# Optimization experiments

Hardware: AMD Instinct MI355X
Metric: run time of the kernel (lower is better)

The kernel has to match this reference:

```python
import jax, jax.numpy as jnp
import numpy as np

N, K, DIM = 65536, 32, 64


def setup_inputs() -> dict:
    key = jax.random.key(0)
    k1, k2, k3, k4 = jax.random.split(key, 4)
    x = jax.random.normal(k1, (N, DIM), jnp.float32)
    log_pi = jax.random.normal(k2, (K, 1), jnp.float32)
    mu = jax.random.normal(k3, (K, DIM), jnp.float32)
    log_sigma_ = jax.random.normal(k4, (K, DIM, DIM), jnp.float32) / 100.0
    return {"x": x, "log_pi": log_pi, "mu": mu, "log_sigma_": log_sigma_}


def reference(x, log_pi, mu, log_sigma_):
    k, d = mu.shape
    # Faithful to torch: softmax over the size-1 last axis of (K,1) -> all ones.
    pi = jax.nn.softmax(log_pi, axis=-1)  # (K, 1)
    # scale_tril construction: strict lower triangle kept, diagonal -> exp(diag) + 1e-3
    diag = jnp.exp(jnp.diagonal(log_sigma_, axis1=-2, axis2=-1)) + 1e-3  # (K, d)
    L = jnp.tril(log_sigma_, -1) + jnp.eye(d, dtype=x.dtype) * diag[:, None, :]  # (K, d, d)
    # batched MVN log_prob via triangular solve
    diff = x[:, None, :] - mu[None, :, :]            # (N, K, d)
    b = jnp.transpose(diff, (1, 2, 0))               # (K, d, N)
    z = jax.scipy.linalg.solve_triangular(L, b, lower=True)  # (K, d, N)
    maha = jnp.sum(z * z, axis=1)                    # (K, N)
    logdet = jnp.sum(jnp.log(diag), axis=-1)         # (K,)
    logp = -0.5 * (maha + d * jnp.log(2.0 * jnp.pi)) - logdet[:, None]  # (K, N)
    p = jnp.exp(logp).T                              # (N, K)
    return jnp.log(jnp.matmul(p, pi).squeeze())      # (N,)
```

## Files before the change

### kernel.cpp

```cpp
#include <hip/hip_runtime.h>

#define KK 32
#define DD 64
#define NB 65536
#define PAD 68
#define FRAGS 12
#define SLOT (FRAGS * 64)
#define MREF 103.0f

typedef __attribute__((ext_vector_type(8))) short bf16x8;
typedef __attribute__((ext_vector_type(4))) float f32x4;

__device__ inline short f2bf(float f) {
  uint32_t u = __builtin_bit_cast(uint32_t, f);
  uint32_t r = (u + 0x7fffu + ((u >> 16) & 1u)) >> 16;
  return (short)(r & 0xffffu);
}
__device__ inline float bf2f(short h) {
  uint32_t u = ((uint32_t)(unsigned short)h) << 16;
  return __builtin_bit_cast(float, u);
}
__device__ inline uint4 pack8(const short* v) {
  uint4 u;
  u.x = (uint32_t)(unsigned short)v[0] | ((uint32_t)(unsigned short)v[1] << 16);
  u.y = (uint32_t)(unsigned short)v[2] | ((uint32_t)(unsigned short)v[3] << 16);
  u.z = (uint32_t)(unsigned short)v[4] | ((uint32_t)(unsigned short)v[5] << 16);
  u.w = (uint32_t)(unsigned short)v[6] | ((uint32_t)(unsigned short)v[7] << 16);
  return u;
}

__global__ __launch_bounds__(64) void md_prep(const float* __restrict__ ls,
                                              const float* __restrict__ mu,
                                              uint4* __restrict__ Bp,
                                              float* __restrict__ Cc,
                                              float* __restrict__ Kc) {
  __shared__ float Ls[DD * DD];
  __shared__ float Ys[DD * PAD];
  const int k = blockIdx.x, j = threadIdx.x;
  const float* __restrict__ lsk = ls + (size_t)k * DD * DD;

#pragma unroll
  for (int it = 0; it < 16; ++it) {
    const int off = it * 256 + j * 4;
    *(float4*)&Ls[off] = *(const float4*)&lsk[off];
  }
  __syncthreads();

  const float dj = expf(Ls[j * DD + j]) + 1e-3f;
  const float invdj = 1.0f / dj;
  {
    float l = logf(dj);
#pragma unroll
    for (int off = 32; off > 0; off >>= 1) l += __shfl_down(l, off, 64);
    if (j == 0) Kc[k] = fmaf(-0.5f, 64.0f * 1.83787706640934534f, -l);
  }

  float z[DD];
#pragma unroll
  for (int i = 0; i < DD; ++i) {
    float s0 = 0.f, s1 = 0.f, s2 = 0.f, s3 = 0.f;
    int m = 0;
#pragma unroll
    for (; m + 4 <= i; m += 4) {
      const float4 lv = *(const float4*)&Ls[i * DD + m];
      s0 = fmaf(lv.x, z[m + 0], s0);
      s1 = fmaf(lv.y, z[m + 1], s1);
      s2 = fmaf(lv.z, z[m + 2], s2);
      s3 = fmaf(lv.w, z[m + 3], s3);
    }
#pragma unroll
    for (; m < i; ++m) s0 = fmaf(Ls[i * DD + m], z[m], s0);
    const float s = (s0 + s1) + (s2 + s3);
    const float di = __shfl(invdj, i, 64);
    z[i] = (i == j) ? invdj : -s * di;
  }

#pragma unroll
  for (int i = 0; i < DD; ++i) Ys[i * PAD + j] = z[i];
  __syncthreads();

  {
    const float* __restrict__ mk = mu + k * DD;
    float c0 = 0.f, c1 = 0.f, c2 = 0.f, c3 = 0.f;
#pragma unroll
    for (int m = 0; m < DD; m += 4) {
      c0 = fmaf(Ys[j * PAD + m + 0], mk[m + 0], c0);
      c1 = fmaf(Ys[j * PAD + m + 1], mk[m + 1], c1);
      c2 = fmaf(Ys[j * PAD + m + 2], mk[m + 2], c2);
      c3 = fmaf(Ys[j * PAD + m + 3], mk[m + 3], c3);
    }
    Cc[k * DD + j] = (c0 + c1) + (c2 + c3);
  }

  const int col = j & 15, q = j >> 4;
  uint4* slot = Bp + (size_t)k * SLOT;
#pragma unroll
  for (int s = 0; s < 2; ++s) {
#pragma unroll
    for (int ct = 0; ct < 4; ++ct) {
      if (s == 1 && ct < 2) continue;
      const int i = col + 16 * ct;
      const float4 v0 = *(const float4*)&Ys[i * PAD + s * 32 + q * 8];
      const float4 v1 = *(const float4*)&Ys[i * PAD + s * 32 + q * 8 + 4];
      const float f[8] = {v0.x, v0.y, v0.z, v0.w, v1.x, v1.y, v1.z, v1.w};
      short hh[8], ll[8];
#pragma unroll
      for (int jj = 0; jj < 8; ++jj) {
        const short h = f2bf(f[jj]);
        hh[jj] = h;
        ll[jj] = f2bf(f[jj] - bf2f(h));
      }
      const int fi = 2 * ct + (s ? 4 : 0);
      slot[(fi + 0) * 64 + j] = pack8(hh);
      slot[(fi + 1) * 64 + j] = pack8(ll);
    }
  }
}

__global__ __launch_bounds__(256, 2) void md_main(const float* __restrict__ x,
                                                  const uint4* __restrict__ Bp,
                                                  const float* __restrict__ Cc,
                                                  const float* __restrict__ Kc,
                                                  float* __restrict__ P) {
  const int tid = threadIdx.x, lane = tid & 63, w = tid >> 6;
  const int quarter = blockIdx.x & 3;
  const int sblk = blockIdx.x >> 2;
  const int base = sblk * 256 + w * 64;
  const int k0 = quarter * 8;
  const int col = lane & 15, q = lane >> 4;

  bf16x8 Xh[4][2], Xl[4][2];
#pragma unroll
  for (int Bt = 0; Bt < 4; ++Bt) {
#pragma unroll
    for (int s = 0; s < 2; ++s) {
      const float* src = x + (size_t)(base + Bt * 16 + col) * DD + s * 32 + q * 8;
      const float4 v0 = *(const float4*)src;
      const float4 v1 = *(const float4*)(src + 4);
      const float f[8] = {v0.x, v0.y, v0.z, v0.w, v1.x, v1.y, v1.z, v1.w};
      bf16x8 h, l;
#pragma unroll
      for (int jj = 0; jj < 8; ++jj) {
        const short hb = f2bf(f[jj]);
        h[jj] = hb;
        l[jj] = f2bf(f[jj] - bf2f(hb));
      }
      Xh[Bt][s] = h;
      Xl[Bt][s] = l;
    }
  }

  const uint4* __restrict__ Bl = Bp + (size_t)k0 * SLOT + lane;

  uint4 F0[FRAGS], F1[FRAGS];
#pragma unroll
  for (int fi = 0; fi < FRAGS; ++fi) F0[fi] = Bl[fi * 64];

  float run_s[4] = {0.f, 0.f, 0.f, 0.f};

#pragma unroll
  for (int kk = 0; kk < 8; ++kk) {
    const int k = k0 + kk;
    const uint4* cur = (kk & 1) ? F1 : F0;
    uint4* nxt = (kk & 1) ? F0 : F1;
    if (kk < 7) {
      const uint4* __restrict__ src = Bl + (size_t)(kk + 1) * SLOT;
#pragma unroll
      for (int fi = 0; fi < FRAGS; ++fi) nxt[fi] = src[fi * 64];
    }
    const float kc = Kc[k];

    f32x4 mah[4];
#pragma unroll
    for (int Bt = 0; Bt < 4; ++Bt) mah[Bt] = (f32x4){0.f, 0.f, 0.f, 0.f};

#pragma unroll
    for (int ct = 0; ct < 4; ++ct) {
      const bf16x8 A0h = __builtin_bit_cast(bf16x8, cur[2 * ct + 0]);
      const bf16x8 A0l = __builtin_bit_cast(bf16x8, cur[2 * ct + 1]);
      bf16x8 A1h{}, A1l{};
      if (ct >= 2) {
        A1h = __builtin_bit_cast(bf16x8, cur[2 * ct + 4]);
        A1l = __builtin_bit_cast(bf16x8, cur[2 * ct + 5]);
      }
      const f32x4 ci = -*(const f32x4*)&Cc[k * DD + ct * 16 + q * 4];
#pragma unroll
      for (int Bt = 0; Bt < 4; ++Bt) {
        f32x4 z1 = ci;
        z1 = __builtin_amdgcn_mfma_f32_16x16x32_bf16(A0h, Xh[Bt][0], z1, 0, 0, 0);
        z1 = __builtin_amdgcn_mfma_f32_16x16x32_bf16(A0l, Xh[Bt][0], z1, 0, 0, 0);
        z1 = __builtin_amdgcn_mfma_f32_16x16x32_bf16(A0h, Xl[Bt][0], z1, 0, 0, 0);
        if (ct >= 2) {
          f32x4 z2 = (f32x4){0.f, 0.f, 0.f, 0.f};
          z2 = __builtin_amdgcn_mfma_f32_16x16x32_bf16(A1h, Xh[Bt][1], z2, 0, 0, 0);
          z2 = __builtin_amdgcn_mfma_f32_16x16x32_bf16(A1l, Xh[Bt][1], z2, 0, 0, 0);
          z2 = __builtin_amdgcn_mfma_f32_16x16x32_bf16(A1h, Xl[Bt][1], z2, 0, 0, 0);
          z1 += z2;
        }
        mah[Bt] += z1 * z1;
      }
    }

#pragma unroll
    for (int Bt = 0; Bt < 4; ++Bt) {
      float s = (mah[Bt][0] + mah[Bt][1]) + (mah[Bt][2] + mah[Bt][3]);
      s += __shfl_xor(s, 16, 64);
      s += __shfl_xor(s, 32, 64);
      const float t = fmaf(-0.5f, s, kc);
      run_s[Bt] += __expf(t + MREF);
    }
  }

  if (q == 0) {
#pragma unroll
    for (int Bt = 0; Bt < 4; ++Bt) {
      const int sid = base + Bt * 16 + col;
      P[quarter * NB + sid] = run_s[Bt];
    }
  }
}

__global__ __launch_bounds__(256) void md_comb(const float* __restrict__ P,
                                               float* __restrict__ out) {
  const int n = blockIdx.x * 256 + threadIdx.x;
  const float S = (P[n] + P[NB + n]) + (P[2 * NB + n] + P[3 * NB + n]);
  out[n] = logf(S) - MREF;
}

extern "C" void kernel_launch(void* const* d_in, const int* in_sizes, int n_in,
                              void* d_out, int out_size, void* d_ws, size_t ws_size,
                              hipStream_t stream) {
  const float* x  = (const float*)d_in[0];
  const float* mu = (const float*)d_in[2];
  const float* ls = (const float*)d_in[3];
  float* out = (float*)d_out;

  char* ws = (char*)d_ws;
  uint4* Bp = (uint4*)ws;
  float* Cc = (float*)(ws + (size_t)KK * SLOT * 16);
  float* Kc = Cc + KK * DD;
  float* P  = Kc + KK;

  md_prep<<<KK, DD, 0, stream>>>(ls, mu, Bp, Cc, Kc);
  md_main<<<1024, 256, 0, stream>>>(x, Bp, Cc, Kc, P);
  md_comb<<<NB / 256, 256, 0, stream>>>(P, out);
}
```

Before: 122.2 us.

## Fuse combine into main via atomic counter, expand Mahalanobis with cross term

The separate combine kernel is removed. The last of the four quarter-blocks per sample tile, found through an atomic counter, now sums the partials and writes the log. The mean term is moved out of the per-component MFMA accumulation: a precomputed W = L^-T L^-1 mu cross term is computed once per tile with MFMA, and a constant absorbs mu'Sigma^-1 mu. The prep kernel is widened to 256 threads with a 4-way split of the triangular solve, and waves stagger the order in which they visit components. This removes one launch and the Cc loads, but adds atomics, fences, shuffles, and a cancellation risk in the expanded quadratic form.

New measurement: 268.2 us. +119.5%, slower.

```diff
diff --git a/kernel.cpp b/kernel.cpp
--- a/kernel.cpp
+++ b/kernel.cpp
@@ -29,99 +29,128 @@
   return u;
 }
 
-__global__ __launch_bounds__(64) void md_prep(const float* __restrict__ ls,
-                                              const float* __restrict__ mu,
-                                              uint4* __restrict__ Bp,
-                                              float* __restrict__ Cc,
-                                              float* __restrict__ Kc) {
+__global__ __launch_bounds__(256) void md_prep(const float* __restrict__ ls,
+                                               const float* __restrict__ mu,
+                                               uint4* __restrict__ Bp,
+                                               short* __restrict__ Whp,
+                                               short* __restrict__ Wlp,
+                                               float* __restrict__ Kc2,
+                                               int* __restrict__ cnt) {
   __shared__ float Ls[DD * DD];
   __shared__ float Ys[DD * PAD];
-  const int k = blockIdx.x, j = threadIdx.x;
+  __shared__ float invdL[DD];
+  __shared__ float muL[DD];
+  __shared__ float cL[DD];
+  const int k = blockIdx.x, t = threadIdx.x;
+  const int j = t >> 2, sub = t & 3;
   const float* __restrict__ lsk = ls + (size_t)k * DD * DD;
 
 #pragma unroll
-  for (int it = 0; it < 16; ++it) {
-    const int off = it * 256 + j * 4;
-    *(float4*)&Ls[off] = *(const float4*)&lsk[off];
-  }
-  __syncthreads();
-
-  const float dj = expf(Ls[j * DD + j]) + 1e-3f;
-  const float invdj = 1.0f / dj;
+  for (int it = 0; it < 4; ++it) {
+    const int o = (it * 256 + t) * 4;
+    *(float4*)&Ls[o] = *(const float4*)&lsk[o];
+  }
+  if (t < DD) muL[t] = mu[k * DD + t];
+  __syncthreads();
+  if (t < DD) invdL[t] = 1.0f / (expf(Ls[t * DD + t]) + 1e-3f);
+  __syncthreads();
+
+  const float invdj = invdL[j];
+  float z[16];
+#pragma unroll
+  for (int mi = 0; mi < 16; ++mi) z[mi] = 0.f;
+#pragma unroll
+  for (int i = 0; i < DD; ++i) {
+    float p = 0.f;
+#pragma unroll
+    for (int mi = 0; mi < 16; ++mi) {
+      if (4 * mi < i) {
+        const int m = 4 * mi + sub;
+        p = fmaf(Ls[i * DD + m], (m < i) ? z[mi] : 0.f, p);
+      }
+    }
+    p += __shfl_xor(p, 1, 64);
+    p += __shfl_xor(p, 2, 64);
+    const float zi = (i == j) ? invdj : -p * invdL[i];
+    if (sub == (i & 3)) z[i >> 2] = zi;
+  }
+#pragma unroll
+  for (int mi = 0; mi < 16; ++mi) Ys[(4 * mi + sub) * PAD + j] = z[mi];
+  __syncthreads();
+
   {
-    float l = logf(dj);
-#pragma unroll
-    for (int off = 32; off > 0; off >>= 1) l += __shfl_down(l, off, 64);
-    if (j == 0) Kc[k] = fmaf(-0.5f, 64.0f * 1.83787706640934534f, -l);
-  }
-
-  float z[DD];
-#pragma unroll
-  for (int i = 0; i < DD; ++i) {
-    float s0 = 0.f, s1 = 0.f, s2 = 0.f, s3 = 0.f;
-    int m = 0;
-#pragma unroll
-    for (; m + 4 <= i; m += 4) {
-      const float4 lv = *(const float4*)&Ls[i * DD + m];
-      s0 = fmaf(lv.x, z[m + 0], s0);
-      s1 = fmaf(lv.y, z[m + 1], s1);
-      s2 = fmaf(lv.z, z[m + 2], s2);
-      s3 = fmaf(lv.w, z[m + 3], s3);
-    }
-#pragma unroll
-    for (; m < i; ++m) s0 = fmaf(Ls[i * DD + m], z[m], s0);
-    const float s = (s0 + s1) + (s2 + s3);
-    const float di = __shfl(invdj, i, 64);
-    z[i] = (i == j) ? invdj : -s * di;
-  }
-
-#pragma unroll
-  for (int i = 0; i < DD; ++i) Ys[i * PAD + j] = z[i];
+    float p = 0.f;
+#pragma unroll
+    for (int mi = 0; mi < 16; ++mi) {
+      const int m = 4 * mi + sub;
+      p = fmaf(Ys[j * PAD + m], muL[m], p);
+    }
+    p += __shfl_xor(p, 1, 64);
+    p += __shfl_xor(p, 2, 64);
+    if (sub == 0) cL[j] = p;
+  }
   __syncthreads();
 
   {
-    const float* __restrict__ mk = mu + k * DD;
-    float c0 = 0.f, c1 = 0.f, c2 = 0.f, c3 = 0.f;
-#pragma unroll
-    for (int m = 0; m < DD; m += 4) {
-      c0 = fmaf(Ys[j * PAD + m + 0], mk[m + 0], c0);
-      c1 = fmaf(Ys[j * PAD + m + 1], mk[m + 1], c1);
-      c2 = fmaf(Ys[j * PAD + m + 2], mk[m + 2], c2);
-      c3 = fmaf(Ys[j * PAD + m + 3], mk[m + 3], c3);
-    }
-    Cc[k * DD + j] = (c0 + c1) + (c2 + c3);
-  }
-
-  const int col = j & 15, q = j >> 4;
-  uint4* slot = Bp + (size_t)k * SLOT;
-#pragma unroll
-  for (int s = 0; s < 2; ++s) {
-#pragma unroll
-    for (int ct = 0; ct < 4; ++ct) {
-      if (s == 1 && ct < 2) continue;
-      const int i = col + 16 * ct;
-      const float4 v0 = *(const float4*)&Ys[i * PAD + s * 32 + q * 8];
-      const float4 v1 = *(const float4*)&Ys[i * PAD + s * 32 + q * 8 + 4];
-      const float f[8] = {v0.x, v0.y, v0.z, v0.w, v1.x, v1.y, v1.z, v1.w};
-      short hh[8], ll[8];
-#pragma unroll
-      for (int jj = 0; jj < 8; ++jj) {
-        const short h = f2bf(f[jj]);
-        hh[jj] = h;
-        ll[jj] = f2bf(f[jj] - bf2f(h));
-      }
-      const int fi = 2 * ct + (s ? 4 : 0);
-      slot[(fi + 0) * 64 + j] = pack8(hh);
-      slot[(fi + 1) * 64 + j] = pack8(ll);
-    }
-  }
+    float p = 0.f;
+#pragma unroll
+    for (int ii = 0; ii < 16; ++ii) {
+      const int i = 4 * ii + sub;
+      p = fmaf(Ys[i * PAD + j], cL[i], p);
+    }
+    p += __shfl_xor(p, 1, 64);
+    p += __shfl_xor(p, 2, 64);
+    if (sub == 0) {
+      const short h = f2bf(p);
+      Whp[k * DD + j] = h;
+      Wlp[k * DD + j] = f2bf(p - bf2f(h));
+    }
+  }
+
+  if (t < DD) {
+    float r = -logf(invdL[t]) + 0.5f * cL[t] * cL[t];
+#pragma unroll
+    for (int off = 32; off > 0; off >>= 1) r += __shfl_down(r, off, 64);
+    if (t == 0) Kc2[k] = MREF - 0.5f * (64.0f * 1.83787706640934534f) - r;
+  }
+
+  if (t < DD) {
+    const int colp = t & 15, qp = t >> 4;
+    uint4* slot = Bp + (size_t)k * SLOT;
+#pragma unroll
+    for (int s = 0; s < 2; ++s) {
+#pragma unroll
+      for (int ct = 0; ct < 4; ++ct) {
+        if (s == 1 && ct < 2) continue;
+        const int i = colp + 16 * ct;
+        const float4 v0 = *(const float4*)&Ys[i * PAD + s * 32 + qp * 8];
+        const float4 v1 = *(const float4*)&Ys[i * PAD + s * 32 + qp * 8 + 4];
+        const float f[8] = {v0.x, v0.y, v0.z, v0.w, v1.x, v1.y, v1.z, v1.w};
+        short hh[8], ll[8];
+#pragma unroll
+        for (int jj = 0; jj < 8; ++jj) {
+          const short h = f2bf(f[jj]);
+          hh[jj] = h;
+          ll[jj] = f2bf(f[jj] - bf2f(h));
+        }
+        const int fi = 2 * ct + (s ? 4 : 0);
+        slot[(fi + 0) * 64 + t] = pack8(hh);
+        slot[(fi + 1) * 64 + t] = pack8(ll);
+      }
+    }
+  }
+  if (k == 0) cnt[t] = 0;
 }
 
 __global__ __launch_bounds__(256, 2) void md_main(const float* __restrict__ x,
                                                   const uint4* __restrict__ Bp,
-                                                  const float* __restrict__ Cc,
-                                                  const float* __restrict__ Kc,
-                                                  float* __restrict__ P) {
+                                                  const short* __restrict__ Whp,
+                                                  const short* __restrict__ Wlp,
+                                                  const float* __restrict__ Kc2,
+                                                  float* __restrict__ P,
+                                                  int* __restrict__ cnt,
+                                                  float* __restrict__ out) {
+  __shared__ int sOld;
   const int tid = threadIdx.x, lane = tid & 63, w = tid >> 6;
   const int quarter = blockIdx.x & 3;
   const int sblk = blockIdx.x >> 2;
@@ -150,25 +179,54 @@
     }
   }
 
-  const uint4* __restrict__ Bl = Bp + (size_t)k0 * SLOT + lane;
+  f32x4 crossD[4];
+  {
+    bf16x8 WhF[2], WlF[2];
+    const int rr = col & 7;
+#pragma unroll
+    for (int s = 0; s < 2; ++s) {
+      const size_t off = (size_t)(k0 + rr) * DD + s * 32 + q * 8;
+      uint4 hv = *(const uint4*)(Whp + off);
+      uint4 lv = *(const uint4*)(Wlp + off);
+      if (col >= 8) { hv = (uint4){0, 0, 0, 0}; lv = (uint4){0, 0, 0, 0}; }
+      WhF[s] = __builtin_bit_cast(bf16x8, hv);
+      WlF[s] = __builtin_bit_cast(bf16x8, lv);
+    }
+#pragma unroll
+    for (int Bt = 0; Bt < 4; ++Bt) {
+      f32x4 zc = (f32x4){0.f, 0.f, 0.f, 0.f};
+      zc = __builtin_amdgcn_mfma_f32_16x16x32_bf16(WhF[0], Xh[Bt][0], zc, 0, 0, 0);
+      zc = __builtin_amdgcn_mfma_f32_16x16x32_bf16(WlF[0], Xh[Bt][0], zc, 0, 0, 0);
+      zc = __builtin_amdgcn_mfma_f32_16x16x32_bf16(WhF[0], Xl[Bt][0], zc, 0, 0, 0);
+      zc = __builtin_amdgcn_mfma_f32_16x16x32_bf16(WhF[1], Xh[Bt][1], zc, 0, 0, 0);
+      zc = __builtin_amdgcn_mfma_f32_16x16x32_bf16(WlF[1], Xh[Bt][1], zc, 0, 0, 0);
+      zc = __builtin_amdgcn_mfma_f32_16x16x32_bf16(WhF[1], Xl[Bt][1], zc, 0, 0, 0);
+      crossD[Bt] = zc;
+    }
+  }
+
+  const int r0 = (w & 1) * 4;
+  const uint4* __restrict__ Bq = Bp + (size_t)k0 * SLOT + lane;
 
   uint4 F0[FRAGS], F1[FRAGS];
 #pragma unroll
-  for (int fi = 0; fi < FRAGS; ++fi) F0[fi] = Bl[fi * 64];
+  for (int fi = 0; fi < FRAGS; ++fi) F0[fi] = Bq[(size_t)r0 * SLOT + fi * 64];
 
   float run_s[4] = {0.f, 0.f, 0.f, 0.f};
 
 #pragma unroll
   for (int kk = 0; kk < 8; ++kk) {
-    const int k = k0 + kk;
+    const int kkr = (kk + r0) & 7;
+    const int k = k0 + kkr;
     const uint4* cur = (kk & 1) ? F1 : F0;
     uint4* nxt = (kk & 1) ? F0 : F1;
     if (kk < 7) {
-      const uint4* __restrict__ src = Bl + (size_t)(kk + 1) * SLOT;
+      const int kn = (kk + 1 + r0) & 7;
+      const uint4* __restrict__ src = Bq + (size_t)kn * SLOT;
 #pragma unroll
       for (int fi = 0; fi < FRAGS; ++fi) nxt[fi] = src[fi * 64];
     }
-    const float kc = Kc[k];
+    const float kc = Kc2[k];
 
     f32x4 mah[4];
 #pragma unroll
@@ -183,10 +241,9 @@
         A1h = __builtin_bit_cast(bf16x8, cur[2 * ct + 4]);
         A1l = __builtin_bit_cast(bf16x8, cur[2 * ct + 5]);
       }
-      const f32x4 ci = -*(const f32x4*)&Cc[k * DD + ct * 16 + q * 4];
 #pragma unroll
       for (int Bt = 0; Bt < 4; ++Bt) {
-        f32x4 z1 = ci;
+        f32x4 z1 = (f32x4){0.f, 0.f, 0.f, 0.f};
         z1 = __builtin_amdgcn_mfma_f32_16x16x32_bf16(A0h, Xh[Bt][0], z1, 0, 0, 0);
         z1 = __builtin_amdgcn_mfma_f32_16x16x32_bf16(A0l, Xh[Bt][0], z1, 0, 0, 0);
         z1 = __builtin_amdgcn_mfma_f32_16x16x32_bf16(A0h, Xl[Bt][0], z1, 0, 0, 0);
@@ -201,30 +258,38 @@
       }
     }
 
+    const int half16 = ((kk >> 2) + (w & 1)) & 1;
 #pragma unroll
     for (int Bt = 0; Bt < 4; ++Bt) {
       float s = (mah[Bt][0] + mah[Bt][1]) + (mah[Bt][2] + mah[Bt][3]);
       s += __shfl_xor(s, 16, 64);
       s += __shfl_xor(s, 32, 64);
-      const float t = fmaf(-0.5f, s, kc);
-      run_s[Bt] += __expf(t + MREF);
+      const float cv = __shfl(crossD[Bt][kk & 3], half16 * 16 + col, 64);
+      const float tt = fmaf(-0.5f, s, kc + cv);
+      run_s[Bt] += __expf(tt);
     }
   }
 
   if (q == 0) {
 #pragma unroll
-    for (int Bt = 0; Bt < 4; ++Bt) {
-      const int sid = base + Bt * 16 + col;
-      P[quarter * NB + sid] = run_s[Bt];
-    }
-  }
-}
-
-__global__ __launch_bounds__(256) void md_comb(const float* __restrict__ P,
-                                               float* __restrict__ out) {
-  const int n = blockIdx.x * 256 + threadIdx.x;
-  const float S = (P[n] + P[NB + n]) + (P[2 * NB + n] + P[3 * NB + n]);
-  out[n] = logf(S) - MREF;
+    for (int Bt = 0; Bt < 4; ++Bt)
+      __hip_atomic_store(&P[quarter * NB + base + Bt * 16 + col], run_s[Bt],
+                         __ATOMIC_RELAXED, __HIP_MEMORY_SCOPE_AGENT);
+  }
+  __threadfence();
+  __syncthreads();
+  if (tid == 0) sOld = atomicAdd(&cnt[sblk], 1);
+  __syncthreads();
+  if (sOld == 3) {
+    __threadfence();
+    const int n = sblk * 256 + tid;
+    float S = 0.f;
+#pragma unroll
+    for (int qq = 0; qq < 4; ++qq)
+      S += __hip_atomic_load(&P[qq * NB + n], __ATOMIC_RELAXED,
+                             __HIP_MEMORY_SCOPE_AGENT);
+    out[n] = logf(S) - MREF;
+  }
 }
 
 extern "C" void kernel_launch(void* const* d_in, const int* in_sizes, int n_in,
@@ -236,12 +301,13 @@
   float* out = (float*)d_out;
 
   char* ws = (char*)d_ws;
-  uint4* Bp = (uint4*)ws;
-  float* Cc = (float*)(ws + (size_t)KK * SLOT * 16);
-  float* Kc = Cc + KK * DD;
-  float* P  = Kc + KK;
-
-  md_prep<<<KK, DD, 0, stream>>>(ls, mu, Bp, Cc, Kc);
-  md_main<<<1024, 256, 0, stream>>>(x, Bp, Cc, Kc, P);
-  md_comb<<<NB / 256, 256, 0, stream>>>(P, out);
-}
+  uint4* Bp  = (uint4*)ws;
+  float* P   = (float*)(ws + (size_t)KK * SLOT * 16);
+  short* Whp = (short*)(P + 4 * NB);
+  short* Wlp = Whp + KK * DD;
+  float* Kc2 = (float*)(Wlp + KK * DD);
+  int*   cnt = (int*)(Kc2 + KK);
+
+  md_prep<<<KK, 256, 0, stream>>>(ls, mu, Bp, Whp, Wlp, Kc2, cnt);
+  md_main<<<1024, 256, 0, stream>>>(x, Bp, Whp, Wlp, Kc2, P, cnt, out);
+}
```
